# Optimization experiments

Measured on AMD Instinct MI355X. Metric: run time of the kernel, lower is better.

Reference implementation:

```python
import jax, jax.numpy as jnp
import numpy as np

E = 128   # embed_dim
H = 8     # num_heads
N, T, LQ, LK = 32, 50, 64, 64


def setup_inputs() -> dict:
    rng = jax.random.key(0)
    ks = jax.random.split(rng, 9)
    xav = np.sqrt(2.0 / (E + E)).astype(np.float32)  # xavier_normal for square E x E
    return {
        "query": jax.random.normal(ks[0], (N, T, LQ, E), jnp.float32),
        "key": jax.random.normal(ks[1], (N, T, LK, E), jnp.float32),
        "value": jax.random.normal(ks[2], (N, T, LK, E), jnp.float32),
        "key_padding_mask": jax.random.bernoulli(ks[3], 0.1, (N, T, LK)),
        "Wq": jax.random.normal(ks[4], (E, E), jnp.float32) * xav,
        "bq": jnp.zeros((E,), jnp.float32),
        "Wk": jax.random.normal(ks[5], (E, E), jnp.float32) * xav,
        "bk": jnp.zeros((E,), jnp.float32),
        "Wv": jax.random.normal(ks[6], (E, E), jnp.float32) * xav,
        "bv": jnp.zeros((E,), jnp.float32),
        "Wo": jax.random.normal(ks[7], (E, E), jnp.float32) * xav,
        "bo": jnp.zeros((E,), jnp.float32),
    }


def reference(query, key, value, key_padding_mask, Wq, bq, Wk, bk, Wv, bv, Wo, bo):
    b, t, lq, _ = query.shape
    lk = key.shape[2]
    # linear projections (torch Linear: x @ W.T + b)
    q = (query @ Wq.T + bq).reshape(b, t, lq, H, -1)   # [b,T,Lq,h,d]
    k = (key @ Wk.T + bk).reshape(b, t, lk, H, -1)     # [b,T,Lk,h,d]
    v = (value @ Wv.T + bv).reshape(b, t, lk, H, -1)   # [b,T,Lk,h,d]
    scale = 1.0 / np.sqrt(q.shape[-1]).astype(np.float32)
    attn = jnp.einsum('bTlhd,bTthd->bThlt', q, k) * scale  # [b,T,h,Lq,Lk]
    mask = key_padding_mask[:, :, None, None, :]            # [b,T,1,1,Lk]
    attn = jnp.where(mask, -jnp.inf, attn)
    attn = jax.nn.softmax(attn, axis=-1)
    attn = jnp.nan_to_num(attn, nan=0.0)                    # fully-masked rows -> 0
    out = jnp.einsum('bThlt,bTthd->bTlhd', attn, v)
    out = out.reshape(b, t, lq, -1) @ Wo.T + bo             # [b,T,Lq,E]
    # match torch output layout for attn: [head, b, T, Lq, Lk]
    return out, jnp.transpose(attn, (2, 0, 1, 3, 4))
```

## Files before the change

kernel.cpp:

```cpp
#include <hip/hip_runtime.h>
#include <hip/hip_bf16.h>


#define NBT 1600
#define OUT0_ELEMS 13107200L

typedef __attribute__((ext_vector_type(8))) short bf16x8;
typedef __attribute__((ext_vector_type(4))) short bf16x4;
typedef __attribute__((ext_vector_type(4))) float f32x4;
typedef __attribute__((ext_vector_type(4))) unsigned short u16x4;

__device__ __forceinline__ unsigned short f2b(float f) {
  union { float f; unsigned u; } v; v.f = f;
  unsigned r = v.u + 0x7FFFu + ((v.u >> 16) & 1u);
  return (unsigned short)(r >> 16);
}
__device__ __forceinline__ float b2f(unsigned short s) {
  union { unsigned u; float f; } v; v.u = ((unsigned)s) << 16;
  return v.f;
}
__device__ __forceinline__ bf16x4 pack4(f32x4 v) {
  bf16x4 r;
  r[0] = (short)f2b(v[0]); r[1] = (short)f2b(v[1]);
  r[2] = (short)f2b(v[2]); r[3] = (short)f2b(v[3]);
  return r;
}

#if defined(__has_builtin)
#if __has_builtin(__builtin_amdgcn_mfma_f32_16x16x16bf16_1k)
#define HAVE_MFMA16_1K 1
#endif
#endif

__device__ __forceinline__ f32x4 mfma16(bf16x4 a, bf16x4 b, f32x4 c) {
#ifdef HAVE_MFMA16_1K
  return __builtin_amdgcn_mfma_f32_16x16x16bf16_1k(a, b, c, 0, 0, 0);
#else
  f32x4 d;
  asm volatile("v_mfma_f32_16x16x16_bf16 %0, %1, %2, %3\n\ts_nop 7\n\ts_nop 7"
               : "=v"(d)
               : "v"(a), "v"(b), "v"(c));
  return d;
#endif
}

__global__ void detect_mask_mode(const unsigned char* __restrict__ p,
                                 int* __restrict__ flag) {
  __shared__ int sb, sf;
  int t = threadIdx.x;
  if (t == 0) { sb = 0; sf = 0; }
  __syncthreads();
  int bnz = 0, fcnt = 0;
  for (int i = t * 16; i < t * 16 + 16; ++i)
    if ((i & 3) && p[i]) bnz++;
  const unsigned int* w = (const unsigned int*)p;
  for (int i = t * 4; i < t * 4 + 4; ++i)
    if (w[i] == 0x3f800000u) fcnt++;
  if (bnz) atomicAdd(&sb, 1);
  if (fcnt) atomicAdd(&sf, 1);
  __syncthreads();
  if (t == 0) *flag = sf ? 2 : (sb ? 1 : 0);
}

__global__ void prep_weights(const float* __restrict__ Wq,
                             const float* __restrict__ Wk,
                             const float* __restrict__ Wv,
                             const float* __restrict__ Wo,
                             unsigned short* __restrict__ wall) {
  int idx = blockIdx.x * 256 + threadIdx.x;
  int m = idx >> 14, j = idx & 16383;
  const float* src = (m == 0) ? Wq : (m == 1) ? Wk : (m == 2) ? Wv : Wo;
  float s = (m == 0) ? 0.25f : 1.0f;
  wall[idx] = f2b(src[j] * s);
}

__global__ __launch_bounds__(512, 4) void fused_kernel(
    const float* __restrict__ q_in, const float* __restrict__ k_in,
    const float* __restrict__ v_in, const unsigned char* __restrict__ maskp,
    const int* __restrict__ modeFlag, const unsigned short* __restrict__ wall,
    const float* __restrict__ bq, const float* __restrict__ bk,
    const float* __restrict__ bv, const float* __restrict__ bo,
    float* __restrict__ out0, float* __restrict__ attn_out) {
  __shared__ __align__(16) unsigned short Ksh[8][64][24];
  __shared__ __align__(16) unsigned short Qbuf[8 * 64 * 24];
  __shared__ __align__(16) unsigned short Xs[64][136];
  __shared__ float maskS[64];

  auto Qsh = (unsigned short(*)[64][24])Qbuf;
  auto Oh  = (unsigned short(*)[136])Qbuf;

  const int tid = threadIdx.x;
  const int w = tid >> 6;
  const int lane = tid & 63;
  const int ln = lane & 15, g = lane >> 4;
  const long bT = blockIdx.x;

  if (tid < 64) {
    int mode = *modeFlag;
    long midx = bT * 64 + tid;
    bool mk;
    if (mode == 0)      mk = ((const int*)maskp)[midx] != 0;
    else if (mode == 1) mk = maskp[midx] != 0;
    else                mk = ((const float*)maskp)[midx] != 0.0f;
    maskS[tid] = mk ? -INFINITY : 0.0f;
  }

  float4 xr[3][4];
  {
    const float* xs0 = q_in + bT * 8192;
    const float* xs1 = k_in + bT * 8192;
    const float* xs2 = v_in + bT * 8192;
    #pragma unroll
    for (int it = 0; it < 4; ++it) {
      int flat = it * 2048 + tid * 4;
      xr[0][it] = *(const float4*)(xs0 + flat);
      xr[1][it] = *(const float4*)(xs1 + flat);
      xr[2][it] = *(const float4*)(xs2 + flat);
    }
  }

  bf16x4 vk[4];

  #pragma unroll
  for (int t3 = 0; t3 < 3; ++t3) {
    #pragma unroll
    for (int it = 0; it < 4; ++it) {
      int flat = it * 2048 + tid * 4;
      int r = flat >> 7, c = flat & 127;
      float4 xv = xr[t3][it];
      u16x4 pk;
      pk[0] = f2b(xv.x); pk[1] = f2b(xv.y);
      pk[2] = f2b(xv.z); pk[3] = f2b(xv.w);
      *(u16x4*)&Xs[r][c] = pk;
    }
    __syncthreads();

    const unsigned short* wb = wall + t3 * 16384 + (w * 16 + ln) * 128 + 8 * g;
    bf16x8 bw[4];
    #pragma unroll
    for (int ks = 0; ks < 4; ++ks) bw[ks] = *(const bf16x8*)(wb + ks * 32);
    const float* bias = (t3 == 0) ? bq : (t3 == 1) ? bk : bv;
    float bval = bias[w * 16 + ln] * ((t3 == 0) ? 0.25f : 1.0f);

    f32x4 acc[4] = {};
    #pragma unroll
    for (int ks = 0; ks < 4; ++ks) {
      bf16x8 a[4];
      #pragma unroll
      for (int ms = 0; ms < 4; ++ms)
        a[ms] = *(const bf16x8*)&Xs[ms * 16 + ln][ks * 32 + 8 * g];
      #pragma unroll
      for (int ms = 0; ms < 4; ++ms)
        acc[ms] = __builtin_amdgcn_mfma_f32_16x16x32_bf16(a[ms], bw[ks],
                                                          acc[ms], 0, 0, 0);
    }
    __syncthreads();

    #pragma unroll
    for (int ms = 0; ms < 4; ++ms) {
      if (t3 == 2) {
        f32x4 vb;
        #pragma unroll
        for (int r = 0; r < 4; ++r) vb[r] = acc[ms][r] + bval;
        vk[ms] = pack4(vb);
      } else {
        #pragma unroll
        for (int r = 0; r < 4; ++r) {
          int l = ms * 16 + 4 * g + r;
          unsigned short hv = f2b(acc[ms][r] + bval);
          if (t3 == 0) Qsh[w][l][ln] = hv;
          else         Ksh[w][l][ln] = hv;
        }
      }
    }
  }

  f32x4 s[4][4] = {};
  {
    bf16x4 aK[4], bQ[4];
    #pragma unroll
    for (int i = 0; i < 4; ++i) {
      aK[i] = *(const bf16x4*)&Ksh[w][i * 16 + ln][4 * g];
      bQ[i] = *(const bf16x4*)&Qsh[w][i * 16 + ln][4 * g];
    }
    #pragma unroll
    for (int t = 0; t < 4; ++t)
      #pragma unroll
      for (int l = 0; l < 4; ++l)
        s[t][l] = mfma16(aK[t], bQ[l], s[t][l]);
  }

  float mv[4][4];
  #pragma unroll
  for (int t = 0; t < 4; ++t)
    #pragma unroll
    for (int r = 0; r < 4; ++r) mv[t][r] = maskS[t * 16 + 4 * g + r];

  #pragma unroll
  for (int l = 0; l < 4; ++l) {
    float m = -INFINITY;
    #pragma unroll
    for (int t = 0; t < 4; ++t)
      #pragma unroll
      for (int r = 0; r < 4; ++r) {
        float sv = s[t][l][r] + mv[t][r];
        s[t][l][r] = sv;
        m = fmaxf(m, sv);
      }
    m = fmaxf(m, __shfl_xor(m, 16, 64));
    m = fmaxf(m, __shfl_xor(m, 32, 64));
    float sum = 0.f;
    #pragma unroll
    for (int t = 0; t < 4; ++t)
      #pragma unroll
      for (int r = 0; r < 4; ++r) {
        float p = (m == -INFINITY) ? 0.f : __expf(s[t][l][r] - m);
        s[t][l][r] = p;
        sum += p;
      }
    sum += __shfl_xor(sum, 16, 64);
    sum += __shfl_xor(sum, 32, 64);
    float inv = (sum > 0.f) ? 1.f / sum : 0.f;
    #pragma unroll
    for (int t = 0; t < 4; ++t)
      #pragma unroll
      for (int r = 0; r < 4; ++r) s[t][l][r] *= inv;
  }

  bf16x4 pa[4][4];
  {
    const long abase = ((long)w * NBT + bT) * 4096;
    #pragma unroll
    for (int lsub = 0; lsub < 4; ++lsub) {
      long rowb = abase + (long)(lsub * 16 + ln) * 64;
      #pragma unroll
      for (int tsub = 0; tsub < 4; ++tsub) {
        *(f32x4*)&attn_out[rowb + tsub * 16 + 4 * g] = s[tsub][lsub];
        pa[tsub][lsub] = pack4(s[tsub][lsub]);
      }
    }
  }

  f32x4 oacc[4] = {};
  #pragma unroll
  for (int lsub = 0; lsub < 4; ++lsub)
    #pragma unroll
    for (int tsub = 0; tsub < 4; ++tsub)
      oacc[lsub] = mfma16(pa[tsub][lsub], vk[tsub], oacc[lsub]);

  __syncthreads();

  #pragma unroll
  for (int lsub = 0; lsub < 4; ++lsub)
    #pragma unroll
    for (int r = 0; r < 4; ++r)
      Oh[lsub * 16 + 4 * g + r][w * 16 + ln] = f2b(oacc[lsub][r]);

  __syncthreads();

  {
    const unsigned short* wo = wall + 3 * 16384 + (w * 16 + ln) * 128 + 8 * g;
    bf16x8 bwo[4];
    #pragma unroll
    for (int ks = 0; ks < 4; ++ks) bwo[ks] = *(const bf16x8*)(wo + ks * 32);
    float bov = bo[w * 16 + ln];

    f32x4 acc[4] = {};
    #pragma unroll
    for (int ks = 0; ks < 4; ++ks) {
      bf16x8 a[4];
      #pragma unroll
      for (int ms = 0; ms < 4; ++ms)
        a[ms] = *(const bf16x8*)&Oh[ms * 16 + ln][ks * 32 + 8 * g];
      #pragma unroll
      for (int ms = 0; ms < 4; ++ms)
        acc[ms] = __builtin_amdgcn_mfma_f32_16x16x32_bf16(a[ms], bwo[ks],
                                                          acc[ms], 0, 0, 0);
    }
    #pragma unroll
    for (int ms = 0; ms < 4; ++ms)
      #pragma unroll
      for (int r = 0; r < 4; ++r)
        out0[(bT * 64 + ms * 16 + 4 * g + r) * 128 + w * 16 + ln] =
            acc[ms][r] + bov;
  }
}

extern "C" void kernel_launch(void* const* d_in, const int* in_sizes, int n_in,
                              void* d_out, int out_size, void* d_ws,
                              size_t ws_size, hipStream_t stream) {
  (void)in_sizes; (void)n_in; (void)out_size; (void)ws_size;
  const float* query = (const float*)d_in[0];
  const float* key   = (const float*)d_in[1];
  const float* value = (const float*)d_in[2];
  const unsigned char* mask = (const unsigned char*)d_in[3];
  const float* Wq = (const float*)d_in[4];
  const float* bq = (const float*)d_in[5];
  const float* Wk = (const float*)d_in[6];
  const float* bk = (const float*)d_in[7];
  const float* Wv = (const float*)d_in[8];
  const float* bv = (const float*)d_in[9];
  const float* Wo = (const float*)d_in[10];
  const float* bo = (const float*)d_in[11];

  float* out0 = (float*)d_out;
  float* attn_out = out0 + OUT0_ELEMS;

  char* ws = (char*)d_ws;
  int* flag = (int*)ws;
  unsigned short* wall = (unsigned short*)(ws + 256);

  detect_mask_mode<<<1, 256, 0, stream>>>(mask, flag);
  prep_weights<<<256, 256, 0, stream>>>(Wq, Wk, Wv, Wo, wall);
  fused_kernel<<<NBT, 512, 0, stream>>>(query, key, value, mask, flag, wall,
                                        bq, bk, bv, bo, out0, attn_out);
}
```

Baseline: 120.9 us.

## Swizzle shared-memory layouts to drop padding, raise occupancy, merge prep kernels

Replaces the padded Xs and Q/K shared arrays with unpadded XOR-swizzled layouts, which cuts LDS per block and avoids bank conflicts, and raises the launch_bounds occupancy hint from 4 to 6. It also merges the mask-detect and weight-prep kernels into a single launch to save one launch. The risk is register pressure from the higher occupancy target, and the Oh alias now overlays the Q/K buffer, so its size and layout must still fit.

```diff
diff --git a/kernel.cpp b/kernel.cpp
--- a/kernel.cpp
+++ b/kernel.cpp
@@ -44,56 +44,66 @@
 #endif
 }
 
-__global__ void detect_mask_mode(const unsigned char* __restrict__ p,
-                                 int* __restrict__ flag) {
-  __shared__ int sb, sf;
+__device__ __forceinline__ int xs_idx(int r, int c) {
+  return r * 128 + (c ^ ((r & 7) << 3));
+}
+__device__ __forceinline__ int qk_idx(int l, int d) {
+  return l * 16 + (d ^ ((l & 3) << 2));
+}
+
+__global__ void prep_kernel(const float* __restrict__ Wq,
+                            const float* __restrict__ Wk,
+                            const float* __restrict__ Wv,
+                            const float* __restrict__ Wo,
+                            const unsigned char* __restrict__ maskp,
+                            unsigned short* __restrict__ wall,
+                            int* __restrict__ flag) {
+  int b = blockIdx.x;
   int t = threadIdx.x;
-  if (t == 0) { sb = 0; sf = 0; }
-  __syncthreads();
-  int bnz = 0, fcnt = 0;
-  for (int i = t * 16; i < t * 16 + 16; ++i)
-    if ((i & 3) && p[i]) bnz++;
-  const unsigned int* w = (const unsigned int*)p;
-  for (int i = t * 4; i < t * 4 + 4; ++i)
-    if (w[i] == 0x3f800000u) fcnt++;
-  if (bnz) atomicAdd(&sb, 1);
-  if (fcnt) atomicAdd(&sf, 1);
-  __syncthreads();
-  if (t == 0) *flag = sf ? 2 : (sb ? 1 : 0);
-}
-
-__global__ void prep_weights(const float* __restrict__ Wq,
-                             const float* __restrict__ Wk,
-                             const float* __restrict__ Wv,
-                             const float* __restrict__ Wo,
-                             unsigned short* __restrict__ wall) {
-  int idx = blockIdx.x * 256 + threadIdx.x;
-  int m = idx >> 14, j = idx & 16383;
-  const float* src = (m == 0) ? Wq : (m == 1) ? Wk : (m == 2) ? Wv : Wo;
-  float s = (m == 0) ? 0.25f : 1.0f;
-  wall[idx] = f2b(src[j] * s);
-}
-
-__global__ __launch_bounds__(512, 4) void fused_kernel(
+  if (b < 256) {
+    int idx = b * 256 + t;
+    int m = idx >> 14, j = idx & 16383;
+    const float* src = (m == 0) ? Wq : (m == 1) ? Wk : (m == 2) ? Wv : Wo;
+    float s = (m == 0) ? 0.25f : 1.0f;
+    wall[idx] = f2b(src[j] * s);
+  } else {
+    __shared__ int sb, sf;
+    if (t == 0) { sb = 0; sf = 0; }
+    __syncthreads();
+    int bnz = 0, fcnt = 0;
+    for (int i = t * 16; i < t * 16 + 16; ++i)
+      if ((i & 3) && maskp[i]) bnz++;
+    const unsigned int* w = (const unsigned int*)maskp;
+    for (int i = t * 4; i < t * 4 + 4; ++i)
+      if (w[i] == 0x3f800000u) fcnt++;
+    if (bnz) atomicAdd(&sb, 1);
+    if (fcnt) atomicAdd(&sf, 1);
+    __syncthreads();
+    if (t == 0) *flag = sf ? 2 : (sb ? 1 : 0);
+  }
+}
+
+__global__ __launch_bounds__(512, 6) void fused_kernel(
     const float* __restrict__ q_in, const float* __restrict__ k_in,
     const float* __restrict__ v_in, const unsigned char* __restrict__ maskp,
     const int* __restrict__ modeFlag, const unsigned short* __restrict__ wall,
     const float* __restrict__ bq, const float* __restrict__ bk,
     const float* __restrict__ bv, const float* __restrict__ bo,
     float* __restrict__ out0, float* __restrict__ attn_out) {
-  __shared__ __align__(16) unsigned short Ksh[8][64][24];
-  __shared__ __align__(16) unsigned short Qbuf[8 * 64 * 24];
-  __shared__ __align__(16) unsigned short Xs[64][136];
+  __shared__ __align__(16) unsigned short Xs[64 * 128];
+  __shared__ __align__(16) unsigned short QKbuf[2 * 8192];
   __shared__ float maskS[64];
 
-  auto Qsh = (unsigned short(*)[64][24])Qbuf;
-  auto Oh  = (unsigned short(*)[136])Qbuf;
+  auto Oh = (unsigned short(*)[136])QKbuf;
 
   const int tid = threadIdx.x;
   const int w = tid >> 6;
   const int lane = tid & 63;
   const int ln = lane & 15, g = lane >> 4;
   const long bT = blockIdx.x;
+
+  unsigned short* Qw = QKbuf + w * 1024;
+  unsigned short* Kw = QKbuf + 8192 + w * 1024;
 
   if (tid < 64) {
     int mode = *modeFlag;
@@ -131,7 +141,7 @@
       u16x4 pk;
       pk[0] = f2b(xv.x); pk[1] = f2b(xv.y);
       pk[2] = f2b(xv.z); pk[3] = f2b(xv.w);
-      *(u16x4*)&Xs[r][c] = pk;
+      *(u16x4*)&Xs[xs_idx(r, c)] = pk;
     }
     __syncthreads();
 
@@ -148,7 +158,7 @@
       bf16x8 a[4];
       #pragma unroll
       for (int ms = 0; ms < 4; ++ms)
-        a[ms] = *(const bf16x8*)&Xs[ms * 16 + ln][ks * 32 + 8 * g];
+        a[ms] = *(const bf16x8*)&Xs[xs_idx(ms * 16 + ln, ks * 32 + 8 * g)];
       #pragma unroll
       for (int ms = 0; ms < 4; ++ms)
         acc[ms] = __builtin_amdgcn_mfma_f32_16x16x32_bf16(a[ms], bw[ks],
@@ -164,12 +174,11 @@
         for (int r = 0; r < 4; ++r) vb[r] = acc[ms][r] + bval;
         vk[ms] = pack4(vb);
       } else {
+        unsigned short* dst = (t3 == 0) ? Qw : Kw;
         #pragma unroll
         for (int r = 0; r < 4; ++r) {
           int l = ms * 16 + 4 * g + r;
-          unsigned short hv = f2b(acc[ms][r] + bval);
-          if (t3 == 0) Qsh[w][l][ln] = hv;
-          else         Ksh[w][l][ln] = hv;
+          dst[qk_idx(l, ln)] = f2b(acc[ms][r] + bval);
         }
       }
     }
@@ -180,8 +189,8 @@
     bf16x4 aK[4], bQ[4];
     #pragma unroll
     for (int i = 0; i < 4; ++i) {
-      aK[i] = *(const bf16x4*)&Ksh[w][i * 16 + ln][4 * g];
-      bQ[i] = *(const bf16x4*)&Qsh[w][i * 16 + ln][4 * g];
+      aK[i] = *(const bf16x4*)&Kw[qk_idx(i * 16 + ln, 4 * g)];
+      bQ[i] = *(const bf16x4*)&Qw[qk_idx(i * 16 + ln, 4 * g)];
     }
     #pragma unroll
     for (int t = 0; t < 4; ++t)
@@ -310,8 +319,7 @@
   int* flag = (int*)ws;
   unsigned short* wall = (unsigned short*)(ws + 256);
 
-  detect_mask_mode<<<1, 256, 0, stream>>>(mask, flag);
-  prep_weights<<<256, 256, 0, stream>>>(Wq, Wk, Wv, Wo, wall);
+  prep_kernel<<<257, 256, 0, stream>>>(Wq, Wk, Wv, Wo, mask, wall, flag);
   fused_kernel<<<NBT, 512, 0, stream>>>(query, key, value, mask, flag, wall,
                                         bq, bk, bv, bo, out0, attn_out);
 }
```

Measured after the change: 166.8 us. 1.38x slower.
